# Optimization experiments

Measured on AMD Instinct MI355X. Metric: run time of the kernel, lower is better.

The kernel has to match this reference:

```python
import jax, jax.numpy as jnp
import numpy as np

B, T, D = 256, 1024, 64          # batch, timesteps, num motor units (input_dim)
H, IC_DIM, F_DIM = 128, 100, 3   # hidden_dim, IC_dim, factors_dim


def setup_inputs() -> dict:
    key = jax.random.key(0)
    ks = jax.random.split(key, 16)
    s = 0.08  # ~1/sqrt(H) scale like torch default init
    f32 = jnp.float32
    return {
        "mu_batch": jax.random.normal(ks[0], (B, T, D), f32),
        # Encoder GRU (input D -> hidden H), PyTorch gate order [r, z, n]
        "We_ih": jax.random.normal(ks[1], (3 * H, D), f32) * s,
        "We_hh": jax.random.normal(ks[2], (3 * H, H), f32) * s,
        "be_ih": jax.random.normal(ks[3], (3 * H,), f32) * s,
        "be_hh": jax.random.normal(ks[4], (3 * H,), f32) * s,
        # IC layer H -> IC_DIM
        "W_ic": jax.random.normal(ks[5], (IC_DIM, H), f32) * s,
        "b_ic": jax.random.normal(ks[6], (IC_DIM,), f32) * s,
        # Generator GRU (input IC_DIM -> hidden H)
        "Wg_ih": jax.random.normal(ks[7], (3 * H, IC_DIM), f32) * s,
        "Wg_hh": jax.random.normal(ks[8], (3 * H, H), f32) * s,
        "bg_ih": jax.random.normal(ks[9], (3 * H,), f32) * s,
        "bg_hh": jax.random.normal(ks[10], (3 * H,), f32) * s,
        # GenToFactors H -> F_DIM
        "W_gf": jax.random.normal(ks[11], (F_DIM, H), f32) * s,
        "b_gf": jax.random.normal(ks[12], (F_DIM,), f32) * s,
        # FactorsToRates F_DIM -> D
        "W_fr": jax.random.normal(ks[13], (D, F_DIM), f32) * s,
        "b_fr": jax.random.normal(ks[14], (D,), f32) * s,
    }


def _gru_step(W_hh, b_hh):
    """PyTorch GRU cell: x_proj = W_ih @ x + b_ih precomputed, gate order r,z,n."""
    def step(h, x_proj):
        gh = h @ W_hh.T + b_hh
        xr, xz, xn = jnp.split(x_proj, 3, axis=-1)
        hr, hz, hn = jnp.split(gh, 3, axis=-1)
        r = jax.nn.sigmoid(xr + hr)
        z = jax.nn.sigmoid(xz + hz)
        n = jnp.tanh(xn + r * hn)
        h_new = (1.0 - z) * n + z * h
        return h_new, h_new
    return step


def reference(mu_batch, We_ih, We_hh, be_ih, be_hh, W_ic, b_ic,
              Wg_ih, Wg_hh, bg_ih, bg_hh, W_gf, b_gf, W_fr, b_fr):
    Bsz, Tlen, _ = mu_batch.shape
    Hdim = We_hh.shape[1]
    h0 = jnp.zeros((Bsz, Hdim), mu_batch.dtype)

    # ----- Encoder GRU: only final hidden state is used -----
    x_proj = jnp.einsum('btd,gd->btg', mu_batch, We_ih) + be_ih   # [B,T,3H]
    h_enc, _ = jax.lax.scan(_gru_step(We_hh, be_hh), h0,
                            jnp.swapaxes(x_proj, 0, 1))           # [B,H]

    # ----- IC layer -----
    IC = h_enc @ W_ic.T + b_ic                                    # [B,IC]

    # ----- Generator GRU: constant input IC fed for T steps, init hidden = h_enc -----
    ic_proj = IC @ Wg_ih.T + bg_ih                                # [B,3H], constant per step
    gstep = _gru_step(Wg_hh, bg_hh)
    def gen_step(h, _):
        return gstep(h, ic_proj)
    _, gen_out = jax.lax.scan(gen_step, h_enc, None, length=Tlen) # [T,B,H]
    gen_out = jnp.swapaxes(gen_out, 0, 1)                         # [B,T,H] == full_gen_out

    # ----- Readout -----
    factors = jnp.einsum('bth,fh->btf', gen_out, W_gf) + b_gf     # [B,T,F]
    rates = jnp.einsum('btf,df->btd', jnp.exp(factors), W_fr) + b_fr  # [B,T,D]
    return rates
```

## Files before the change

kernel.cpp:

```cpp
#include <hip/hip_runtime.h>
#include <hip/hip_bf16.h>

#define Bn 256
#define Tn 1024
#define Dn 64
#define Hn 128
#define G3 384
#define ICn 100
#define BT 16
#define NTH 512
#define LDH 136
#define LDX 72

typedef _Float16 f16;
typedef __attribute__((ext_vector_type(8))) _Float16 f16x8;
typedef __attribute__((ext_vector_type(4))) _Float16 f16x4;
typedef __attribute__((ext_vector_type(4))) float f32x4;

#define MFMA(a, b, c) __builtin_amdgcn_mfma_f32_16x16x32_f16((a), (b), (c), 0, 0, 0)

#define S_SIG  (-1.4426950408889634f)
#define S_TANH (-2.8853900817779268f)
#define S_EXP  ( 1.4426950408889634f)

__device__ __forceinline__ float rcpa(float x) { return __builtin_amdgcn_rcpf(x); }
__device__ __forceinline__ float ex2(float x) {
#if __has_builtin(__builtin_amdgcn_exp2f)
    return __builtin_amdgcn_exp2f(x);
#else
    return exp2f(x);
#endif
}
__device__ __forceinline__ float sigm2(float x) { return rcpa(1.0f + ex2(x)); }
__device__ __forceinline__ float tanh2(float x) { return fmaf(2.0f, rcpa(1.0f + ex2(x)), -1.0f); }

__device__ __forceinline__ f16x8 ldw(const float* W, int row, int ldk, int k0, float s) {
    const float* p = W + (size_t)row * ldk + k0;
    f16x8 r;
#pragma unroll
    for (int j = 0; j < 8; ++j) r[j] = (f16)(p[j] * s);
    return r;
}

__global__ __launch_bounds__(NTH, 2)
void enc_kernel(const float* __restrict__ mu,
                const float* __restrict__ We_ih, const float* __restrict__ We_hh,
                const float* __restrict__ be_ih, const float* __restrict__ be_hh,
                float* __restrict__ h_enc)
{
    const int b0 = blockIdx.x * BT;
    const int tid = threadIdx.x;
    const int w = tid >> 6, l = tid & 63, c = l & 15, q = l >> 4;

    __shared__ f16 hbuf[2][BT * LDH];
    __shared__ f16 xstg[2][8][BT * LDX];

    const int gr = w * 16 + c, gz = Hn + w * 16 + c, gn = 2 * Hn + w * 16 + c;

    f16x8 whf[3][4], wxf[3][2];
#pragma unroll
    for (int kt = 0; kt < 4; ++kt) {
        whf[0][kt] = ldw(We_hh, gr, Hn, kt * 32 + q * 8, S_SIG);
        whf[1][kt] = ldw(We_hh, gz, Hn, kt * 32 + q * 8, S_SIG);
        whf[2][kt] = ldw(We_hh, gn, Hn, kt * 32 + q * 8, S_TANH);
    }
#pragma unroll
    for (int kt = 0; kt < 2; ++kt) {
        wxf[0][kt] = ldw(We_ih, gr, Dn, kt * 32 + q * 8, S_SIG);
        wxf[1][kt] = ldw(We_ih, gz, Dn, kt * 32 + q * 8, S_SIG);
        wxf[2][kt] = ldw(We_ih, gn, Dn, kt * 32 + q * 8, S_TANH);
    }
    const float brc = S_SIG * (be_ih[gr] + be_hh[gr]);
    const float bzc = S_SIG * (be_ih[gz] + be_hh[gz]);
    const float bxn = S_TANH * be_ih[gn];
    const float bhn = S_TANH * be_hh[gn];

    float hreg[4];
#pragma unroll
    for (int r4 = 0; r4 < 4; ++r4) hreg[r4] = 0.0f;
    for (int i = tid; i < BT * Hn; i += NTH) hbuf[0][(i >> 7) * LDH + (i & 127)] = (f16)0.0f;

    const int SIT = (BT * 8 * Dn) / (NTH * 4);
#pragma unroll
    for (int i = 0; i < SIT; ++i) {
        int f = (i * NTH + tid) * 4;
        int t_off = f >> 10, rem = f & 1023;
        int bb = rem >> 6, d = rem & 63;
        const float4 v = *reinterpret_cast<const float4*>(
            mu + ((size_t)(b0 + bb) * Tn + t_off) * Dn + d);
        f16x4 h4; h4[0] = (f16)v.x; h4[1] = (f16)v.y; h4[2] = (f16)v.z; h4[3] = (f16)v.w;
        *reinterpret_cast<f16x4*>(&xstg[0][t_off][bb * LDX + d]) = h4;
    }
    __syncthreads();

    float4 pre[SIT];
    for (int t = 0; t < Tn; ++t) {
        const int ch = t >> 3, s = t & 7, cur = t & 1, sb = ch & 1;
        if (s == 0 && ch + 1 < Tn / 8) {
#pragma unroll
            for (int i = 0; i < SIT; ++i) {
                int f = (i * NTH + tid) * 4;
                int t_off = f >> 10, rem = f & 1023;
                int bb = rem >> 6, d = rem & 63;
                pre[i] = *reinterpret_cast<const float4*>(
                    mu + ((size_t)(b0 + bb) * Tn + (ch + 1) * 8 + t_off) * Dn + d);
            }
        }
        f16x8 ah[4], ax[2];
#pragma unroll
        for (int kt = 0; kt < 4; ++kt)
            ah[kt] = *reinterpret_cast<const f16x8*>(&hbuf[cur][c * LDH + kt * 32 + q * 8]);
#pragma unroll
        for (int kt = 0; kt < 2; ++kt)
            ax[kt] = *reinterpret_cast<const f16x8*>(&xstg[sb][s][c * LDX + kt * 32 + q * 8]);

        f32x4 acc0 = (f32x4){0,0,0,0}, acc1 = (f32x4){0,0,0,0};
        f32x4 acc2 = (f32x4){0,0,0,0}, accx = (f32x4){0,0,0,0};
#pragma unroll
        for (int kt = 0; kt < 4; ++kt) {
            acc0 = MFMA(ah[kt], whf[0][kt], acc0);
            acc1 = MFMA(ah[kt], whf[1][kt], acc1);
            acc2 = MFMA(ah[kt], whf[2][kt], acc2);
        }
#pragma unroll
        for (int kt = 0; kt < 2; ++kt) {
            acc0 = MFMA(ax[kt], wxf[0][kt], acc0);
            acc1 = MFMA(ax[kt], wxf[1][kt], acc1);
            accx = MFMA(ax[kt], wxf[2][kt], accx);
        }
#pragma unroll
        for (int r4 = 0; r4 < 4; ++r4) {
            float rg = sigm2(acc0[r4] + brc);
            float zg = sigm2(acc1[r4] + bzc);
            float hn = acc2[r4] + bhn;
            float xn = accx[r4] + bxn;
            float ng = tanh2(fmaf(rg, hn, xn));
            float hv = fmaf(zg, hreg[r4] - ng, ng);
            hreg[r4] = hv;
            hbuf[cur ^ 1][(q * 4 + r4) * LDH + w * 16 + c] = (f16)hv;
        }
        if (s == 7 && ch + 1 < Tn / 8) {
#pragma unroll
            for (int i = 0; i < SIT; ++i) {
                int f = (i * NTH + tid) * 4;
                int t_off = f >> 10, rem = f & 1023;
                int bb = rem >> 6, d = rem & 63;
                f16x4 h4;
                h4[0] = (f16)pre[i].x; h4[1] = (f16)pre[i].y;
                h4[2] = (f16)pre[i].z; h4[3] = (f16)pre[i].w;
                *reinterpret_cast<f16x4*>(&xstg[sb ^ 1][t_off][bb * LDX + d]) = h4;
            }
        }
        __syncthreads();
    }
#pragma unroll
    for (int r4 = 0; r4 < 4; ++r4)
        h_enc[(size_t)(b0 + q * 4 + r4) * Hn + w * 16 + c] = hreg[r4];
}

__global__ __launch_bounds__(NTH, 2)
void gen_kernel(const float* __restrict__ h_enc,
                const float* __restrict__ W_ic, const float* __restrict__ b_ic,
                const float* __restrict__ Wg_ih, const float* __restrict__ Wg_hh,
                const float* __restrict__ bg_ih, const float* __restrict__ bg_hh,
                const float* __restrict__ W_gf, const float* __restrict__ b_gf,
                const float* __restrict__ W_fr, const float* __restrict__ b_fr,
                float* __restrict__ out)
{
    const int b0 = blockIdx.x * BT;
    const int tid = threadIdx.x;
    const int w = tid >> 6, l = tid & 63, c = l & 15, q = l >> 4;

    __shared__ f16 hbuf[2][BT * LDH];
    __shared__ float hencs[BT][Hn];
    __shared__ float ics[BT][ICn];
    __shared__ float xpcs[BT][G3];
    __shared__ float fredB[2][8][BT][4];

    for (int i = tid; i < BT * Hn; i += NTH)
        hencs[i >> 7][i & 127] = h_enc[(size_t)(b0 + (i >> 7)) * Hn + (i & 127)];
    __syncthreads();

    for (int i = tid; i < BT * ICn; i += NTH) {
        int bb = i / ICn, j = i - bb * ICn;
        float a = b_ic[j];
        const float* wr = W_ic + (size_t)j * Hn;
#pragma unroll 4
        for (int k = 0; k < Hn; ++k) a = fmaf(wr[k], hencs[bb][k], a);
        ics[bb][j] = a;
    }
    __syncthreads();

    for (int i = tid; i < BT * G3; i += NTH) {
        int g = i >> 4, bb = i & 15;
        float a = bg_ih[g];
        const float* wr = Wg_ih + (size_t)g * ICn;
#pragma unroll 4
        for (int k = 0; k < ICn; ++k) a = fmaf(wr[k], ics[bb][k], a);
        xpcs[bb][g] = a;
    }
    for (int i = tid; i < BT * Hn; i += NTH)
        hbuf[0][(i >> 7) * LDH + (i & 127)] = (f16)hencs[i >> 7][i & 127];

    const int gr = w * 16 + c, gz = Hn + w * 16 + c, gn = 2 * Hn + w * 16 + c;

    f16x8 whf[3][4];
#pragma unroll
    for (int kt = 0; kt < 4; ++kt) {
        whf[0][kt] = ldw(Wg_hh, gr, Hn, kt * 32 + q * 8, S_SIG);
        whf[1][kt] = ldw(Wg_hh, gz, Hn, kt * 32 + q * 8, S_SIG);
        whf[2][kt] = ldw(Wg_hh, gn, Hn, kt * 32 + q * 8, S_TANH);
    }
    f16x8 wgff[4];
#pragma unroll
    for (int kt = 0; kt < 4; ++kt) {
        if (c < 3) wgff[kt] = ldw(W_gf, c, Hn, kt * 32 + q * 8, S_EXP);
        else {
            f16x8 z;
#pragma unroll
            for (int j = 0; j < 8; ++j) z[j] = (f16)0.0f;
            wgff[kt] = z;
        }
    }
    const float bgfc = (c < 3) ? S_EXP * b_gf[c] : 0.0f;
    const int d = l;
    const float wfr0 = W_fr[d * 3 + 0], wfr1 = W_fr[d * 3 + 1], wfr2 = W_fr[d * 3 + 2];
    const float bfrd = b_fr[d];
    float* op0 = out + ((size_t)(b0 + w) * Tn) * Dn + d;
    float* op1 = out + ((size_t)(b0 + w + 8) * Tn) * Dn + d;

    float hreg[4];
#pragma unroll
    for (int r4 = 0; r4 < 4; ++r4) hreg[r4] = hencs[q * 4 + r4][w * 16 + c];

    __syncthreads();

    const float bgr = bg_hh[gr], bgz = bg_hh[gz], bhnr = bg_hh[gn];
    float xrc[4], xzc[4], xnc[4];
#pragma unroll
    for (int r4 = 0; r4 < 4; ++r4) {
        int bb = q * 4 + r4;
        xrc[r4] = S_SIG * (xpcs[bb][gr] + bgr);
        xzc[r4] = S_SIG * (xpcs[bb][gz] + bgz);
        xnc[r4] = S_TANH * xpcs[bb][gn];
    }
    const float bhn = S_TANH * bhnr;

    auto step = [&](int t, const f16* hb_r, f16* hb_w) {
        const int slot = t & 7, par = (t >> 3) & 1;
        f16x8 ah[4];
#pragma unroll
        for (int kt = 0; kt < 4; ++kt)
            ah[kt] = *reinterpret_cast<const f16x8*>(&hb_r[c * LDH + kt * 32 + q * 8]);

        f32x4 acc0 = (f32x4){0,0,0,0}, acc1 = (f32x4){0,0,0,0}, acc2 = (f32x4){0,0,0,0};
#pragma unroll
        for (int kt = 0; kt < 4; ++kt) {
            acc0 = MFMA(ah[kt], whf[0][kt], acc0);
            acc1 = MFMA(ah[kt], whf[1][kt], acc1);
            acc2 = MFMA(ah[kt], whf[2][kt], acc2);
        }
        if (w == slot) {
            f32x4 facc = (f32x4){0, 0, 0, 0};
#pragma unroll
            for (int kt = 0; kt < 4; ++kt) facc = MFMA(ah[kt], wgff[kt], facc);
            if (c < 3) {
#pragma unroll
                for (int r4 = 0; r4 < 4; ++r4)
                    fredB[par][slot][q * 4 + r4][c] = ex2(facc[r4] + bgfc);
            }
        }
#pragma unroll
        for (int r4 = 0; r4 < 4; ++r4) {
            float rg = sigm2(acc0[r4] + xrc[r4]);
            float zg = sigm2(acc1[r4] + xzc[r4]);
            float hn = acc2[r4] + bhn;
            float ng = tanh2(fmaf(rg, hn, xnc[r4]));
            float hv = fmaf(zg, hreg[r4] - ng, ng);
            hreg[r4] = hv;
            hb_w[(q * 4 + r4) * LDH + w * 16 + c] = (f16)hv;
        }
        __syncthreads();
        if (slot == 7) {
            const int base_row = (t >> 3) * 8 - 1;
#pragma unroll
            for (int s = 0; s < 8; ++s) {
                const int r = base_row + s;
                if (r >= 0) {
                    const float4 f0 = *reinterpret_cast<const float4*>(&fredB[par][s][w][0]);
                    op0[(size_t)r * Dn] = bfrd + f0.x * wfr0 + f0.y * wfr1 + f0.z * wfr2;
                    const float4 f1 = *reinterpret_cast<const float4*>(&fredB[par][s][w + 8][0]);
                    op1[(size_t)r * Dn] = bfrd + f1.x * wfr0 + f1.y * wfr1 + f1.z * wfr2;
                }
            }
        }
    };

    for (int tt = 0; tt < Tn; tt += 2) {
        step(tt,     hbuf[0], hbuf[1]);
        step(tt + 1, hbuf[1], hbuf[0]);
    }
    if (w == 0) {
        f16x8 ah[4];
#pragma unroll
        for (int kt = 0; kt < 4; ++kt)
            ah[kt] = *reinterpret_cast<const f16x8*>(&hbuf[0][c * LDH + kt * 32 + q * 8]);
        f32x4 facc = (f32x4){0, 0, 0, 0};
#pragma unroll
        for (int kt = 0; kt < 4; ++kt) facc = MFMA(ah[kt], wgff[kt], facc);
        if (c < 3) {
#pragma unroll
            for (int r4 = 0; r4 < 4; ++r4)
                fredB[0][0][q * 4 + r4][c] = ex2(facc[r4] + bgfc);
        }
    }
    __syncthreads();
    {
        const size_t ofs = (size_t)(Tn - 1) * Dn;
        const float4 f0 = *reinterpret_cast<const float4*>(&fredB[0][0][w][0]);
        op0[ofs] = bfrd + f0.x * wfr0 + f0.y * wfr1 + f0.z * wfr2;
        const float4 f1 = *reinterpret_cast<const float4*>(&fredB[0][0][w + 8][0]);
        op1[ofs] = bfrd + f1.x * wfr0 + f1.y * wfr1 + f1.z * wfr2;
    }
}

extern "C" void kernel_launch(void* const* d_in, const int* in_sizes, int n_in,
                              void* d_out, int out_size, void* d_ws, size_t ws_size,
                              hipStream_t stream) {
    const float* mu    = (const float*)d_in[0];
    const float* We_ih = (const float*)d_in[1];
    const float* We_hh = (const float*)d_in[2];
    const float* be_ih = (const float*)d_in[3];
    const float* be_hh = (const float*)d_in[4];
    const float* W_ic  = (const float*)d_in[5];
    const float* b_ic  = (const float*)d_in[6];
    const float* Wg_ih = (const float*)d_in[7];
    const float* Wg_hh = (const float*)d_in[8];
    const float* bg_ih = (const float*)d_in[9];
    const float* bg_hh = (const float*)d_in[10];
    const float* W_gf  = (const float*)d_in[11];
    const float* b_gf  = (const float*)d_in[12];
    const float* W_fr  = (const float*)d_in[13];
    const float* b_fr  = (const float*)d_in[14];

    float* h_enc = (float*)d_ws;
    float* out = (float*)d_out;

    enc_kernel<<<dim3(Bn / BT), dim3(NTH), 0, stream>>>(mu, We_ih, We_hh, be_ih, be_hh, h_enc);
    gen_kernel<<<dim3(Bn / BT), dim3(NTH), 0, stream>>>(h_enc, W_ic, b_ic, Wg_ih, Wg_hh,
                                                        bg_ih, bg_hh, W_gf, b_gf, W_fr, b_fr, out);
}
```

Before: 1.509 ms.

## Seed MFMA accumulators with biases, raise wave priority, repad hidden-state LDS stride

The GRU gate biases are now loaded into the MFMA accumulator initial values, so the per-element bias adds after the matrix multiply disappear in both the encoder and the generator steps. The MFMA chains are wrapped in s_setprio(1)/s_setprio(0) to raise wave priority while the matrix instructions issue. The LDS row stride for the hidden-state buffer changes from 136 to 140 halves to alter the bank-conflict pattern. Together these aim to shorten the serial per-timestep critical path, but the new padding may itself introduce conflicts on the 16-byte reads or the scalar writes.

```diff
diff --git a/kernel.cpp b/kernel.cpp
--- a/kernel.cpp
+++ b/kernel.cpp
@@ -9,7 +9,7 @@
 #define ICn 100
 #define BT 16
 #define NTH 512
-#define LDH 136
+#define LDH 140
 #define LDX 72
 
 typedef _Float16 f16;
@@ -33,6 +33,8 @@
 }
 __device__ __forceinline__ float sigm2(float x) { return rcpa(1.0f + ex2(x)); }
 __device__ __forceinline__ float tanh2(float x) { return fmaf(2.0f, rcpa(1.0f + ex2(x)), -1.0f); }
+
+__device__ __forceinline__ f32x4 splat4(float v) { return (f32x4){v, v, v, v}; }
 
 __device__ __forceinline__ f16x8 ldw(const float* W, int row, int ldk, int k0, float s) {
     const float* p = W + (size_t)row * ldk + k0;
@@ -114,8 +116,9 @@
         for (int kt = 0; kt < 2; ++kt)
             ax[kt] = *reinterpret_cast<const f16x8*>(&xstg[sb][s][c * LDX + kt * 32 + q * 8]);
 
-        f32x4 acc0 = (f32x4){0,0,0,0}, acc1 = (f32x4){0,0,0,0};
-        f32x4 acc2 = (f32x4){0,0,0,0}, accx = (f32x4){0,0,0,0};
+        f32x4 acc0 = splat4(brc), acc1 = splat4(bzc);
+        f32x4 acc2 = splat4(bhn), accx = splat4(bxn);
+        __builtin_amdgcn_s_setprio(1);
 #pragma unroll
         for (int kt = 0; kt < 4; ++kt) {
             acc0 = MFMA(ah[kt], whf[0][kt], acc0);
@@ -128,13 +131,12 @@
             acc1 = MFMA(ax[kt], wxf[1][kt], acc1);
             accx = MFMA(ax[kt], wxf[2][kt], accx);
         }
+        __builtin_amdgcn_s_setprio(0);
 #pragma unroll
         for (int r4 = 0; r4 < 4; ++r4) {
-            float rg = sigm2(acc0[r4] + brc);
-            float zg = sigm2(acc1[r4] + bzc);
-            float hn = acc2[r4] + bhn;
-            float xn = accx[r4] + bxn;
-            float ng = tanh2(fmaf(rg, hn, xn));
+            float rg = sigm2(acc0[r4]);
+            float zg = sigm2(acc1[r4]);
+            float ng = tanh2(fmaf(rg, acc2[r4], accx[r4]));
             float hv = fmaf(zg, hreg[r4] - ng, ng);
             hreg[r4] = hv;
             hbuf[cur ^ 1][(q * 4 + r4) * LDH + w * 16 + c] = (f16)hv;
@@ -236,15 +238,17 @@
     __syncthreads();
 
     const float bgr = bg_hh[gr], bgz = bg_hh[gz], bhnr = bg_hh[gn];
-    float xrc[4], xzc[4], xnc[4];
+    f32x4 xrcv, xzcv;
+    float xnc[4];
 #pragma unroll
     for (int r4 = 0; r4 < 4; ++r4) {
         int bb = q * 4 + r4;
-        xrc[r4] = S_SIG * (xpcs[bb][gr] + bgr);
-        xzc[r4] = S_SIG * (xpcs[bb][gz] + bgz);
+        xrcv[r4] = S_SIG * (xpcs[bb][gr] + bgr);
+        xzcv[r4] = S_SIG * (xpcs[bb][gz] + bgz);
         xnc[r4] = S_TANH * xpcs[bb][gn];
     }
-    const float bhn = S_TANH * bhnr;
+    const f32x4 bhnv = splat4(S_TANH * bhnr);
+    const f32x4 bgfv = splat4(bgfc);
 
     auto step = [&](int t, const f16* hb_r, f16* hb_w) {
         const int slot = t & 7, par = (t >> 3) & 1;
@@ -253,29 +257,30 @@
         for (int kt = 0; kt < 4; ++kt)
             ah[kt] = *reinterpret_cast<const f16x8*>(&hb_r[c * LDH + kt * 32 + q * 8]);
 
-        f32x4 acc0 = (f32x4){0,0,0,0}, acc1 = (f32x4){0,0,0,0}, acc2 = (f32x4){0,0,0,0};
+        f32x4 acc0 = xrcv, acc1 = xzcv, acc2 = bhnv;
+        __builtin_amdgcn_s_setprio(1);
 #pragma unroll
         for (int kt = 0; kt < 4; ++kt) {
             acc0 = MFMA(ah[kt], whf[0][kt], acc0);
             acc1 = MFMA(ah[kt], whf[1][kt], acc1);
             acc2 = MFMA(ah[kt], whf[2][kt], acc2);
         }
+        __builtin_amdgcn_s_setprio(0);
         if (w == slot) {
-            f32x4 facc = (f32x4){0, 0, 0, 0};
+            f32x4 facc = bgfv;
 #pragma unroll
             for (int kt = 0; kt < 4; ++kt) facc = MFMA(ah[kt], wgff[kt], facc);
             if (c < 3) {
 #pragma unroll
                 for (int r4 = 0; r4 < 4; ++r4)
-                    fredB[par][slot][q * 4 + r4][c] = ex2(facc[r4] + bgfc);
+                    fredB[par][slot][q * 4 + r4][c] = ex2(facc[r4]);
             }
         }
 #pragma unroll
         for (int r4 = 0; r4 < 4; ++r4) {
-            float rg = sigm2(acc0[r4] + xrc[r4]);
-            float zg = sigm2(acc1[r4] + xzc[r4]);
-            float hn = acc2[r4] + bhn;
-            float ng = tanh2(fmaf(rg, hn, xnc[r4]));
+            float rg = sigm2(acc0[r4]);
+            float zg = sigm2(acc1[r4]);
+            float ng = tanh2(fmaf(rg, acc2[r4], xnc[r4]));
             float hv = fmaf(zg, hreg[r4] - ng, ng);
             hreg[r4] = hv;
             hb_w[(q * 4 + r4) * LDH + w * 16 + c] = (f16)hv;
@@ -305,13 +310,13 @@
 #pragma unroll
         for (int kt = 0; kt < 4; ++kt)
             ah[kt] = *reinterpret_cast<const f16x8*>(&hbuf[0][c * LDH + kt * 32 + q * 8]);
-        f32x4 facc = (f32x4){0, 0, 0, 0};
+        f32x4 facc = bgfv;
 #pragma unroll
         for (int kt = 0; kt < 4; ++kt) facc = MFMA(ah[kt], wgff[kt], facc);
         if (c < 3) {
 #pragma unroll
             for (int r4 = 0; r4 < 4; ++r4)
-                fredB[0][0][q * 4 + r4][c] = ex2(facc[r4] + bgfc);
+                fredB[0][0][q * 4 + r4][c] = ex2(facc[r4]);
         }
     }
     __syncthreads();
```

After: 1.992 ms. +32.0%, slower.
